# Performance work log

Measured on AMD Instinct MI355X. Metric: run time of the kernel, lower is better.

The kernel has to match this reference:

```python
import jax, jax.numpy as jnp
import numpy as np

D, H, F, N, V, B, S, T = 512, 8, 2048, 2, 32000, 2, 1024, 1024


def _pe(seq_len, d):
    pos = np.arange(seq_len)[:, None].astype(np.float32)
    div = np.exp(np.arange(0, d, 2).astype(np.float32) * (-np.log(10000.0) / d))
    pe = np.zeros((seq_len, d), np.float32)
    pe[:, 0::2] = np.sin(pos * div)
    pe[:, 1::2] = np.cos(pos * div)
    return jnp.asarray(pe)


def _ln(x, g, b, eps=1e-6):
    # torch .var() default is unbiased (ddof=1)
    m = x.mean(-1, keepdims=True)
    v = jnp.sum((x - m) ** 2, -1, keepdims=True) / (x.shape[-1] - 1)
    return g * (x - m) / jnp.sqrt(v + eps) + b


def _mha(q, k, v, mask, w, b):
    # w: [4, D, D] (q,k,v,o); b: [4, D]
    Bq, Sq, Dm = q.shape
    Sk = k.shape[1]
    dk = Dm // H
    Q = (q @ w[0] + b[0]).reshape(Bq, Sq, H, dk).transpose(0, 2, 1, 3)
    K = (k @ w[1] + b[1]).reshape(Bq, Sk, H, dk).transpose(0, 2, 1, 3)
    Vv = (v @ w[2] + b[2]).reshape(Bq, Sk, H, dk).transpose(0, 2, 1, 3)
    s = jnp.einsum('bhqd,bhkd->bhqk', Q, K) / jnp.sqrt(jnp.float32(dk))
    s = jnp.where(mask == 0, jnp.float32(-1e9), s)
    a = jax.nn.softmax(s, axis=-1)
    o = jnp.einsum('bhqk,bhkd->bhqd', a, Vv).transpose(0, 2, 1, 3).reshape(Bq, Sq, Dm)
    return o @ w[3] + b[3]


def _ffn(x, w1, b1, w2, b2):
    return jax.nn.relu(x @ w1 + b1) @ w2 + b2


def _forward(src, tgt, src_mask, tgt_mask, p):
    (src_emb, tgt_emb, ea_w, ea_b, ef_w1, ef_b1, ef_w2, ef_b2, eln_g, eln_b, en_g, en_b,
     ds_w, ds_b, dc_w, dc_b, df_w1, df_b1, df_w2, df_b2, dln_g, dln_b, dn_g, dn_b, pw, pb) = p
    scale = jnp.sqrt(jnp.float32(D))
    # encoder
    x = src_emb[src] * scale + _pe(src.shape[1], D)
    for i in range(N):
        h = _ln(x, eln_g[i, 0], eln_b[i, 0])
        x = x + _mha(h, h, h, src_mask, ea_w[i], ea_b[i])
        h = _ln(x, eln_g[i, 1], eln_b[i, 1])
        x = x + _ffn(h, ef_w1[i], ef_b1[i], ef_w2[i], ef_b2[i])
    enc = _ln(x, en_g, en_b)
    # decoder
    y = tgt_emb[tgt] * scale + _pe(tgt.shape[1], D)
    for i in range(N):
        h = _ln(y, dln_g[i, 0], dln_b[i, 0])
        y = y + _mha(h, h, h, tgt_mask, ds_w[i], ds_b[i])
        h = _ln(y, dln_g[i, 1], dln_b[i, 1])
        y = y + _mha(h, enc, enc, src_mask, dc_w[i], dc_b[i])
        h = _ln(y, dln_g[i, 2], dln_b[i, 2])
        y = y + _ffn(h, df_w1[i], df_b1[i], df_w2[i], df_b2[i])
    y = _ln(y, dn_g, dn_b)
    return jax.nn.log_softmax(y @ pw + pb, axis=-1)


def setup_inputs() -> dict:
    key = jax.random.key(0)
    c = [0]
    def nk():
        c[0] += 1
        return jax.random.fold_in(key, c[0])
    def w(*s):
        return jax.random.normal(nk(), s, jnp.float32) * 0.02
    inp = {
        'src': jax.random.randint(nk(), (B, S), 0, V, jnp.int32),
        'tgt': jax.random.randint(nk(), (B, T), 0, V, jnp.int32),
        'src_mask': jnp.ones((B, 1, 1, S), jnp.int32),
        'tgt_mask': jnp.tril(jnp.ones((T, T), jnp.int32))[None, None],
        'src_emb': w(V, D), 'tgt_emb': w(V, D),
        'enc_attn_w': w(N, 4, D, D), 'enc_attn_b': jnp.zeros((N, 4, D), jnp.float32),
        'enc_ffn_w1': w(N, D, F), 'enc_ffn_b1': jnp.zeros((N, F), jnp.float32),
        'enc_ffn_w2': w(N, F, D), 'enc_ffn_b2': jnp.zeros((N, D), jnp.float32),
        'enc_ln_g': jnp.ones((N, 2, D), jnp.float32), 'enc_ln_b': jnp.zeros((N, 2, D), jnp.float32),
        'enc_norm_g': jnp.ones((D,), jnp.float32), 'enc_norm_b': jnp.zeros((D,), jnp.float32),
        'dec_self_w': w(N, 4, D, D), 'dec_self_b': jnp.zeros((N, 4, D), jnp.float32),
        'dec_cross_w': w(N, 4, D, D), 'dec_cross_b': jnp.zeros((N, 4, D), jnp.float32),
        'dec_ffn_w1': w(N, D, F), 'dec_ffn_b1': jnp.zeros((N, F), jnp.float32),
        'dec_ffn_w2': w(N, F, D), 'dec_ffn_b2': jnp.zeros((N, D), jnp.float32),
        'dec_ln_g': jnp.ones((N, 3, D), jnp.float32), 'dec_ln_b': jnp.zeros((N, 3, D), jnp.float32),
        'dec_norm_g': jnp.ones((D,), jnp.float32), 'dec_norm_b': jnp.zeros((D,), jnp.float32),
        'proj_w': w(D, V), 'proj_b': jnp.zeros((V,), jnp.float32),
    }
    return inp


def reference(src, tgt, src_mask, tgt_mask, src_emb, tgt_emb, enc_attn_w, enc_attn_b,
              enc_ffn_w1, enc_ffn_b1, enc_ffn_w2, enc_ffn_b2, enc_ln_g, enc_ln_b,
              enc_norm_g, enc_norm_b, dec_self_w, dec_self_b, dec_cross_w, dec_cross_b,
              dec_ffn_w1, dec_ffn_b1, dec_ffn_w2, dec_ffn_b2, dec_ln_g, dec_ln_b,
              dec_norm_g, dec_norm_b, proj_w, proj_b):
    p = (src_emb, tgt_emb, enc_attn_w, enc_attn_b, enc_ffn_w1, enc_ffn_b1, enc_ffn_w2,
         enc_ffn_b2, enc_ln_g, enc_ln_b, enc_norm_g, enc_norm_b, dec_self_w, dec_self_b,
         dec_cross_w, dec_cross_b, dec_ffn_w1, dec_ffn_b1, dec_ffn_w2, dec_ffn_b2,
         dec_ln_g, dec_ln_b, dec_norm_g, dec_norm_b, proj_w, proj_b)
    return _forward(src, tgt, src_mask, tgt_mask, p)
```

## Files before the change

### kernel.cpp

```cpp
#include <hip/hip_runtime.h>
#include <hip/hip_bf16.h>
#include <math.h>

using bf16 = __hip_bfloat16;
typedef float f32x4 __attribute__((ext_vector_type(4)));
typedef short short8 __attribute__((ext_vector_type(8)));

constexpr int kD = 512, kH = 8, kDk = 64, kF = 2048, kV = 32000;
constexpr int kB = 2, kS = 1024, kM = 2048, kBH = 16;

enum { ST_F32 = 0, ST_BF16, ST_QHEAD, ST_QKV, ST_KV };

__device__ __forceinline__ void gload_lds16(const void* g, void* l) {
  __builtin_amdgcn_global_load_lds(
      (const __attribute__((address_space(1))) void*)g,
      (__attribute__((address_space(3))) void*)l, 16, 0, 0);
}

template <int BM, int BN, int STM, bool BIAS, bool RELU, bool RES, bool DBUF, bool XSWZ>
__launch_bounds__(256)
__global__ void k_gemm(const bf16* __restrict__ A, int lda, long long Az,
                       const bf16* __restrict__ Bt, int ldb, long long Bz,
                       void* __restrict__ Cv, int ldc, long long Cz,
                       int K, float alpha,
                       const float* __restrict__ bias,
                       const float* __restrict__ res) {
  static_assert(!DBUF || (BM == 64 && BN == 64), "DBUF path sized for 64x64 (vmcnt(4))");
  constexpr int FM = BM / 32, FN = BN / 32;
  constexpr int NB = DBUF ? 2 : 1;
  __shared__ __attribute__((aligned(16))) bf16 As[NB][BM * 64];
  __shared__ __attribute__((aligned(16))) bf16 Bs[NB][BN * 64];
  const int tid = threadIdx.x;
  const int w = tid >> 6, lane = tid & 63;
  int bx = blockIdx.x, by = blockIdx.y;
  if constexpr (XSWZ) {
    const int nx = gridDim.x;
    const int lin = by * nx + bx;
    const int cpx = (nx * gridDim.y) >> 3;
    const int s = (lin & 7) * cpx + (lin >> 3);
    bx = s % nx;
    by = s / nx;
  }
  const int bm = by * BM, bn = bx * BN;
  const int z = blockIdx.z;
  A += (long long)z * Az;
  Bt += (long long)z * Bz;
  const int l15 = lane & 15, lhi = lane >> 4;
  const int wr = (w >> 1) * (BM / 2), wc = (w & 1) * (BN / 2);
  f32x4 acc[FM][FN] = {};
  const int nkt = K >> 6;

  auto stage = [&](int kt, int nb) {
#pragma unroll
    for (int it = 0; it < BM / 32; ++it) {
      int chunk = (it * 4 + w) * 64 + lane;
      int row = chunk >> 3, col = (chunk & 7) << 3;
      gload_lds16(A + (size_t)(bm + row) * lda + kt * 64 + col, As[nb] + (it * 4 + w) * 512);
    }
#pragma unroll
    for (int it = 0; it < BN / 32; ++it) {
      int chunk = (it * 4 + w) * 64 + lane;
      int row = chunk >> 3, col = (chunk & 7) << 3;
      gload_lds16(Bt + (size_t)(bn + row) * ldb + kt * 64 + col, Bs[nb] + (it * 4 + w) * 512);
    }
  };
  auto compute = [&](int cb) {
#pragma unroll
    for (int kk = 0; kk < 2; ++kk) {
      short8 af[FM], bf[FN];
#pragma unroll
      for (int i = 0; i < FM; ++i)
        af[i] = *(const short8*)(As[cb] + (wr + i * 16 + l15) * 64 + kk * 32 + lhi * 8);
#pragma unroll
      for (int j = 0; j < FN; ++j)
        bf[j] = *(const short8*)(Bs[cb] + (wc + j * 16 + l15) * 64 + kk * 32 + lhi * 8);
#pragma unroll
      for (int i = 0; i < FM; ++i)
#pragma unroll
        for (int j = 0; j < FN; ++j)
          acc[i][j] = __builtin_amdgcn_mfma_f32_16x16x32_bf16(af[i], bf[j], acc[i][j], 0, 0, 0);
    }
  };

  if constexpr (DBUF) {
    stage(0, 0);
    stage(1, 1);
    asm volatile("s_waitcnt vmcnt(4)" ::: "memory");
    __builtin_amdgcn_s_barrier();
    __builtin_amdgcn_sched_barrier(0);
    int cur = 0;
    for (int kt = 0; kt < nkt; ++kt) {
      compute(cur);
      asm volatile("s_waitcnt lgkmcnt(0)" ::: "memory");
      __builtin_amdgcn_sched_barrier(0);
      if (kt + 1 < nkt) {
        __builtin_amdgcn_s_barrier();
        if (kt + 2 < nkt) {
          stage(kt + 2, cur);
          asm volatile("s_waitcnt vmcnt(4)" ::: "memory");
        } else {
          asm volatile("s_waitcnt vmcnt(0)" ::: "memory");
        }
        __builtin_amdgcn_s_barrier();
        __builtin_amdgcn_sched_barrier(0);
      }
      cur ^= 1;
    }
  } else {
    for (int kt = 0; kt < nkt; ++kt) {
      stage(kt, 0);
      __syncthreads();
      compute(0);
      __syncthreads();
    }
  }

#pragma unroll
  for (int i = 0; i < FM; ++i) {
#pragma unroll
    for (int j = 0; j < FN; ++j) {
#pragma unroll
      for (int r = 0; r < 4; ++r) {
        int m = bm + wr + i * 16 + lhi * 4 + r;
        int n = bn + wc + j * 16 + l15;
        float val = acc[i][j][r] * alpha;
        if constexpr (BIAS) val += bias[n];
        if constexpr (RELU) val = fmaxf(val, 0.f);
        if constexpr (RES) val += res[(size_t)m * ldc + n];
        if constexpr (STM == ST_F32) {
          ((float*)Cv)[(size_t)z * Cz + (size_t)m * ldc + n] = val;
        } else if constexpr (STM == ST_BF16) {
          ((bf16*)Cv)[(size_t)z * Cz + (size_t)m * ldc + n] = __float2bfloat16(val);
        } else if constexpr (STM == ST_QHEAD) {
          int b_ = m >> 10, s_ = m & 1023, h_ = n >> 6, d_ = n & 63;
          ((bf16*)Cv)[(((size_t)(b_ * kH + h_) << 10) + s_) * kDk + d_] = __float2bfloat16(val);
        } else if constexpr (STM == ST_QKV) {
          int seg = n >> 9, nn = n & 511;
          int b_ = m >> 10, s_ = m & 1023, h_ = nn >> 6, d_ = nn & 63;
          size_t idx = (seg < 2)
              ? (((size_t)(b_ * kH + h_) << 10) + s_) * kDk + d_
              : ((size_t)(b_ * kH + h_) * kDk + d_) * kS + s_;
          ((bf16*)Cv)[(size_t)seg * 1048576 + idx] = __float2bfloat16(val);
        } else if constexpr (STM == ST_KV) {
          int seg = n >> 9, nn = n & 511;
          int b_ = m >> 10, s_ = m & 1023, h_ = nn >> 6, d_ = nn & 63;
          size_t idx = (seg == 0)
              ? (((size_t)(b_ * kH + h_) << 10) + s_) * kDk + d_
              : ((size_t)(b_ * kH + h_) * kDk + d_) * kS + s_;
          ((bf16*)Cv)[(size_t)(seg + 1) * 1048576 + idx] = __float2bfloat16(val);
        }
      }
    }
  }
}

template <bool CAUSAL>
__launch_bounds__(256)
__global__ void k_fattn(const bf16* __restrict__ Q, const bf16* __restrict__ K,
                        const bf16* __restrict__ Vt, bf16* __restrict__ O) {
  __shared__ __attribute__((aligned(16))) bf16 Ks[2][4096];
  __shared__ __attribute__((aligned(16))) bf16 Vs[2][4096];
  __shared__ __attribute__((aligned(16))) bf16 Ps[4][1024];
  const int tid = threadIdx.x, w = tid >> 6, lane = tid & 63;
  const int l15 = lane & 15, lhi = lane >> 4;
  const int q0 = blockIdx.x * 64, bh = blockIdx.y;
  const int qw = q0 + w * 16;
  const bf16* Qp = Q + (((size_t)(bh << 10)) + qw + l15) * kDk;
  short8 aq[2];
  aq[0] = *(const short8*)(Qp + lhi * 8);
  aq[1] = *(const short8*)(Qp + 32 + lhi * 8);
  const int srow = w * 8 + (lane >> 3);
  const int sc = (lane & 7) ^ (srow & 7);
  const bf16* Ksrc = K + (((size_t)(bh << 10)) + srow) * kDk + sc * 8;
  const bf16* Vsrc = Vt + ((size_t)bh * kDk + srow) * kS + sc * 8;
  const int nt = CAUSAL ? (q0 >> 6) + 1 : (kS >> 6);

  auto stage = [&](int t, int nb) {
    int kv0 = t << 6;
    gload_lds16(Ksrc + (size_t)kv0 * kDk, Ks[nb] + w * 512);
    gload_lds16(Ksrc + (size_t)(kv0 + 32) * kDk, Ks[nb] + 2048 + w * 512);
    gload_lds16(Vsrc + kv0, Vs[nb] + w * 512);
    gload_lds16(Vsrc + kv0 + 32 * kS, Vs[nb] + 2048 + w * 512);
  };

  float m_[4], l_[4];
#pragma unroll
  for (int r = 0; r < 4; ++r) { m_[r] = -1e30f; l_[r] = 0.f; }
  f32x4 ao[4] = {};

  stage(0, 0);
  if (nt > 1) {
    stage(1, 1);
    asm volatile("s_waitcnt vmcnt(4)" ::: "memory");
  } else {
    asm volatile("s_waitcnt vmcnt(0)" ::: "memory");
  }
  __builtin_amdgcn_s_barrier();
  __builtin_amdgcn_sched_barrier(0);

  for (int t = 0; t < nt; ++t) {
    const int cur = t & 1;
    f32x4 as[4] = {};
#pragma unroll
    for (int kk = 0; kk < 2; ++kk) {
      short8 bk[4];
#pragma unroll
      for (int nf = 0; nf < 4; ++nf) {
        int row = nf * 16 + l15;
        int c = (4 * kk + lhi) ^ (row & 7);
        bk[nf] = *(const short8*)(Ks[cur] + row * 64 + c * 8);
      }
#pragma unroll
      for (int nf = 0; nf < 4; ++nf)
        as[nf] = __builtin_amdgcn_mfma_f32_16x16x32_bf16(aq[kk], bk[nf], as[nf], 0, 0, 0);
    }
    float s[4][4];
#pragma unroll
    for (int nf = 0; nf < 4; ++nf)
#pragma unroll
      for (int r = 0; r < 4; ++r) {
        float v = as[nf][r] * 0.125f;
        if (CAUSAL && t == nt - 1) {
          int col = (t << 6) + nf * 16 + l15;
          int row = qw + lhi * 4 + r;
          if (col > row) v = -1e30f;
        }
        s[nf][r] = v;
      }
    float mn[4], scl[4], rsum[4];
#pragma unroll
    for (int r = 0; r < 4; ++r) {
      float mx = fmaxf(fmaxf(s[0][r], s[1][r]), fmaxf(s[2][r], s[3][r]));
      mx = fmaxf(mx, __shfl_xor(mx, 1));
      mx = fmaxf(mx, __shfl_xor(mx, 2));
      mx = fmaxf(mx, __shfl_xor(mx, 4));
      mx = fmaxf(mx, __shfl_xor(mx, 8));
      mn[r] = fmaxf(m_[r], mx);
      scl[r] = __expf(m_[r] - mn[r]);
      rsum[r] = 0.f;
    }
#pragma unroll
    for (int nf = 0; nf < 4; ++nf)
#pragma unroll
      for (int r = 0; r < 4; ++r) {
        float p = __expf(s[nf][r] - mn[r]);
        rsum[r] += p;
        int pr = lhi * 4 + r;
        int c = (2 * nf + (l15 >> 3)) ^ (pr & 7);
        Ps[w][pr * 64 + c * 8 + (l15 & 7)] = __float2bfloat16(p);
      }
#pragma unroll
    for (int r = 0; r < 4; ++r) {
      float su = rsum[r];
      su += __shfl_xor(su, 1);
      su += __shfl_xor(su, 2);
      su += __shfl_xor(su, 4);
      su += __shfl_xor(su, 8);
      l_[r] = l_[r] * scl[r] + su;
      m_[r] = mn[r];
    }
#pragma unroll
    for (int nf = 0; nf < 4; ++nf)
#pragma unroll
      for (int r = 0; r < 4; ++r) ao[nf][r] *= scl[r];
    asm volatile("s_waitcnt lgkmcnt(0)" ::: "memory");
    __builtin_amdgcn_sched_barrier(0);
#pragma unroll
    for (int kk = 0; kk < 2; ++kk) {
      short8 pa = *(const short8*)(Ps[w] + l15 * 64 + (((4 * kk + lhi) ^ (l15 & 7)) * 8));
      short8 bv[4];
#pragma unroll
      for (int nf = 0; nf < 4; ++nf) {
        int row = nf * 16 + l15;
        int c = (4 * kk + lhi) ^ (row & 7);
        bv[nf] = *(const short8*)(Vs[cur] + row * 64 + c * 8);
      }
#pragma unroll
      for (int nf = 0; nf < 4; ++nf)
        ao[nf] = __builtin_amdgcn_mfma_f32_16x16x32_bf16(pa, bv[nf], ao[nf], 0, 0, 0);
    }
    asm volatile("s_waitcnt lgkmcnt(0)" ::: "memory");
    __builtin_amdgcn_sched_barrier(0);
    if (t + 1 < nt) {
      __builtin_amdgcn_s_barrier();
      if (t + 2 < nt) {
        stage(t + 2, cur);
        asm volatile("s_waitcnt vmcnt(4)" ::: "memory");
      } else {
        asm volatile("s_waitcnt vmcnt(0)" ::: "memory");
      }
      __builtin_amdgcn_s_barrier();
      __builtin_amdgcn_sched_barrier(0);
    }
  }
  const int b_ = bh >> 3, h_ = bh & 7;
  float inv[4];
#pragma unroll
  for (int r = 0; r < 4; ++r) inv[r] = 1.f / l_[r];
#pragma unroll
  for (int nf = 0; nf < 4; ++nf)
#pragma unroll
    for (int r = 0; r < 4; ++r) {
      int q = qw + lhi * 4 + r;
      O[((size_t)(b_ * kS + q)) * kD + h_ * kDk + nf * 16 + l15] =
          __float2bfloat16(ao[nf][r] * inv[r]);
    }
}

struct TJobs {
  const float* src[8];
  bf16* dst[8];
  int K[8], N[8];
  int ofs[9];
};

__global__ void k_transpose_all(TJobs J) {
  __shared__ float t[32][33];
  const int tb = blockIdx.x;
  int j = 0;
#pragma unroll
  for (int i = 1; i < 8; ++i) j += (tb >= J.ofs[i]) ? 1 : 0;
  const int K = J.K[j], N = J.N[j];
  const int tn = N >> 5, tk = K >> 5;
  int r = tb - J.ofs[j];
  const int z = r / (tn * tk);
  r -= z * tn * tk;
  const int k0 = (r / tn) << 5, n0 = (r % tn) << 5;
  const float* Wp = J.src[j] + (size_t)z * K * N;
  bf16* WTp = J.dst[j] + (size_t)z * K * N;
  const int tx = threadIdx.x, ty = threadIdx.y;
#pragma unroll
  for (int rr = 0; rr < 32; rr += 8) t[ty + rr][tx] = Wp[(size_t)(k0 + ty + rr) * N + n0 + tx];
  __syncthreads();
#pragma unroll
  for (int rr = 0; rr < 32; rr += 8)
    WTp[(size_t)(n0 + ty + rr) * K + k0 + tx] = __float2bfloat16(t[tx][ty + rr]);
}

__global__ void k_embed(const int* __restrict__ tok, const float* __restrict__ emb,
                        float* __restrict__ x) {
  int m = blockIdx.x;
  int s = m & (kS - 1);
  const float* e = emb + (size_t)tok[m] * kD;
  float* xp = x + (size_t)m * kD;
  for (int d = threadIdx.x; d < kD; d += 256) {
    int i = d >> 1;
    float freq = __expf(-(float)(2 * i) * (9.210340371976184f / 512.0f));
    float ang = (float)s * freq;
    float pe = (d & 1) ? cosf(ang) : sinf(ang);
    xp[d] = e[d] * 22.62741699796952f + pe;
  }
}

__global__ void k_ln(const float* __restrict__ x, const float* __restrict__ g,
                     const float* __restrict__ b, bf16* __restrict__ out) {
  int w = threadIdx.x >> 6, lane = threadIdx.x & 63;
  int row = blockIdx.x * 4 + w;
  const float* xp = x + (size_t)row * kD;
  float v[8];
  float sum = 0.f;
#pragma unroll
  for (int i = 0; i < 8; ++i) { v[i] = xp[lane + i * 64]; sum += v[i]; }
#pragma unroll
  for (int o = 32; o; o >>= 1) sum += __shfl_xor(sum, o);
  float mean = sum * (1.f / 512.f);
  float sq = 0.f;
#pragma unroll
  for (int i = 0; i < 8; ++i) { float d = v[i] - mean; sq += d * d; }
#pragma unroll
  for (int o = 32; o; o >>= 1) sq += __shfl_xor(sq, o);
  float inv = rsqrtf(sq * (1.f / 511.f) + 1e-6f);
  bf16* op = out + (size_t)row * kD;
#pragma unroll
  for (int i = 0; i < 8; ++i) {
    int d = lane + i * 64;
    op[d] = __float2bfloat16(g[d] * (v[i] - mean) * inv + b[d]);
  }
}

__global__ __launch_bounds__(640, 2) void k_logsoftmax(float* __restrict__ y) {
  float* row = y + (size_t)blockIdx.x * kV;
  const int t = threadIdx.x;
  float v[50];
  float mx = -1e30f;
#pragma unroll
  for (int i = 0; i < 50; ++i) { v[i] = row[t + i * 640]; mx = fmaxf(mx, v[i]); }
#pragma unroll
  for (int o = 32; o; o >>= 1) mx = fmaxf(mx, __shfl_xor(mx, o));
  __shared__ float red[10], red2[10];
  const int w = t >> 6, lane = t & 63;
  if (lane == 0) red[w] = mx;
  __syncthreads();
#pragma unroll
  for (int i = 0; i < 10; ++i) mx = fmaxf(mx, red[i]);
  float sum = 0.f;
#pragma unroll
  for (int i = 0; i < 50; ++i) { v[i] -= mx; sum += __expf(v[i]); }
#pragma unroll
  for (int o = 32; o; o >>= 1) sum += __shfl_xor(sum, o);
  if (lane == 0) red2[w] = sum;
  __syncthreads();
  sum = 0.f;
#pragma unroll
  for (int i = 0; i < 10; ++i) sum += red2[i];
  const float ls = logf(sum);
#pragma unroll
  for (int i = 0; i < 50; ++i) row[t + i * 640] = v[i] - ls;
}

extern "C" void kernel_launch(void* const* d_in, const int* in_sizes, int n_in,
                              void* d_out, int out_size, void* d_ws, size_t ws_size,
                              hipStream_t stream) {
  (void)in_sizes; (void)n_in; (void)out_size;
  if (ws_size < (size_t)80 * 1024 * 1024) return;

  const int* src = (const int*)d_in[0];
  const int* tgt = (const int*)d_in[1];
  const float* src_emb   = (const float*)d_in[4];
  const float* tgt_emb   = (const float*)d_in[5];
  const float* enc_attn_w = (const float*)d_in[6];
  const float* enc_attn_b = (const float*)d_in[7];
  const float* enc_ffn_w1 = (const float*)d_in[8];
  const float* enc_ffn_b1 = (const float*)d_in[9];
  const float* enc_ffn_w2 = (const float*)d_in[10];
  const float* enc_ffn_b2 = (const float*)d_in[11];
  const float* enc_ln_g  = (const float*)d_in[12];
  const float* enc_ln_b  = (const float*)d_in[13];
  const float* enc_norm_g = (const float*)d_in[14];
  const float* enc_norm_b = (const float*)d_in[15];
  const float* dec_self_w = (const float*)d_in[16];
  const float* dec_self_b = (const float*)d_in[17];
  const float* dec_cross_w = (const float*)d_in[18];
  const float* dec_cross_b = (const float*)d_in[19];
  const float* dec_ffn_w1 = (const float*)d_in[20];
  const float* dec_ffn_b1 = (const float*)d_in[21];
  const float* dec_ffn_w2 = (const float*)d_in[22];
  const float* dec_ffn_b2 = (const float*)d_in[23];
  const float* dec_ln_g  = (const float*)d_in[24];
  const float* dec_ln_b  = (const float*)d_in[25];
  const float* dec_norm_g = (const float*)d_in[26];
  const float* dec_norm_b = (const float*)d_in[27];
  const float* proj_w    = (const float*)d_in[28];
  const float* proj_b    = (const float*)d_in[29];

  char* ws = (char*)d_ws;
  auto MB = [](size_t x) { return x << 20; };
  bf16* enc_attn_wt  = (bf16*)(ws + MB(0));
  bf16* dec_self_wt  = (bf16*)(ws + MB(4));
  bf16* dec_cross_wt = (bf16*)(ws + MB(8));
  bf16* enc_f1t = (bf16*)(ws + MB(12));
  bf16* enc_f2t = (bf16*)(ws + MB(16));
  bf16* dec_f1t = (bf16*)(ws + MB(20));
  bf16* dec_f2t = (bf16*)(ws + MB(24));
  bf16* proj_wt = (bf16*)(ws + MB(28));
  float* x_enc  = (float*)(ws + MB(60));
  float* x_dec  = (float*)(ws + MB(64));
  bf16* hbuf    = (bf16*)(ws + MB(68));
  bf16* enc_bf  = (bf16*)(ws + MB(70));
  bf16* Qb      = (bf16*)(ws + MB(72));
  bf16* Kb      = (bf16*)(ws + MB(74));
  bf16* VtB     = (bf16*)(ws + MB(76));
  bf16* attn_o  = (bf16*)(ws + MB(78));
  bf16* ffn_mid = (bf16*)d_out;

  TJobs tj;
  int acc = 0;
  auto setj = [&](int j, const float* s, bf16* d, int K, int N, int z) {
    tj.src[j] = s; tj.dst[j] = d; tj.K[j] = K; tj.N[j] = N; tj.ofs[j] = acc;
    acc += (K >> 5) * (N >> 5) * z;
  };
  setj(0, enc_attn_w, enc_attn_wt, 512, 512, 8);
  setj(1, dec_self_w, dec_self_wt, 512, 512, 8);
  setj(2, dec_cross_w, dec_cross_wt, 512, 512, 8);
  setj(3, enc_ffn_w1, enc_f1t, 512, 2048, 2);
  setj(4, enc_ffn_w2, enc_f2t, 2048, 512, 2);
  setj(5, dec_ffn_w1, dec_f1t, 512, 2048, 2);
  setj(6, dec_ffn_w2, dec_f2t, 2048, 512, 2);
  setj(7, proj_w, proj_wt, 512, 32000, 1);
  tj.ofs[8] = acc;
  k_transpose_all<<<acc, dim3(32, 8), 0, stream>>>(tj);

  k_embed<<<kM, 256, 0, stream>>>(src, src_emb, x_enc);
  k_embed<<<kM, 256, 0, stream>>>(tgt, tgt_emb, x_dec);

  auto LN = [&](const float* x, const float* g, const float* b, bf16* out) {
    k_ln<<<kM / 4, 256, 0, stream>>>(x, g, b, out);
  };
  auto out_proj = [&](const bf16* wt, const float* bias, float* xio) {
    k_gemm<64, 64, ST_F32, true, false, true, true, false><<<dim3(8, 32, 1), 256, 0, stream>>>(
        attn_o, 512, 0, wt + 3 * 262144, 512, 0, xio, 512, 0, 512, 1.f, bias + 3 * 512, xio);
  };
  auto self_attn = [&](const bf16* wt, const float* bias, bool causal, float* xio) {
    k_gemm<64, 64, ST_QKV, true, false, false, true, false><<<dim3(24, 32, 1), 256, 0, stream>>>(
        hbuf, 512, 0, wt, 512, 0, Qb, 0, 0, 512, 1.f, bias, nullptr);
    if (causal) k_fattn<true><<<dim3(16, kBH), 256, 0, stream>>>(Qb, Kb, VtB, attn_o);
    else        k_fattn<false><<<dim3(16, kBH), 256, 0, stream>>>(Qb, Kb, VtB, attn_o);
    out_proj(wt, bias, xio);
  };
  auto cross_attn = [&](const bf16* wt, const float* bias, float* xio) {
    k_gemm<64, 64, ST_QHEAD, true, false, false, true, false><<<dim3(8, 32, 1), 256, 0, stream>>>(
        hbuf, 512, 0, wt, 512, 0, Qb, 0, 0, 512, 1.f, bias, nullptr);
    k_gemm<64, 64, ST_KV, true, false, false, true, false><<<dim3(16, 32, 1), 256, 0, stream>>>(
        enc_bf, 512, 0, wt + 1 * 262144, 512, 0, Qb, 0, 0, 512, 1.f, bias + 512, nullptr);
    k_fattn<false><<<dim3(16, kBH), 256, 0, stream>>>(Qb, Kb, VtB, attn_o);
    out_proj(wt, bias, xio);
  };
  auto ffn_block = [&](float* xio, const bf16* w1t, const float* b1, const bf16* w2t,
                       const float* b2, const float* g, const float* bl) {
    LN(xio, g, bl, hbuf);
    k_gemm<128, 128, ST_BF16, true, true, false, false, false><<<dim3(16, 16, 1), 256, 0, stream>>>(
        hbuf, 512, 0, w1t, 512, 0, ffn_mid, 2048, 0, 512, 1.f, b1, nullptr);
    k_gemm<64, 64, ST_F32, true, false, true, true, false><<<dim3(8, 32, 1), 256, 0, stream>>>(
        ffn_mid, 2048, 0, w2t, 2048, 0, xio, 512, 0, 2048, 1.f, b2, xio);
  };

  for (int i = 0; i < 2; ++i) {
    LN(x_enc, enc_ln_g + i * 1024, enc_ln_b + i * 1024, hbuf);
    self_attn(enc_attn_wt + (size_t)i * 1048576, enc_attn_b + i * 2048, false, x_enc);
    ffn_block(x_enc, enc_f1t + (size_t)i * 1048576, enc_ffn_b1 + i * 2048,
              enc_f2t + (size_t)i * 1048576, enc_ffn_b2 + i * 512,
              enc_ln_g + i * 1024 + 512, enc_ln_b + i * 1024 + 512);
  }
  LN(x_enc, enc_norm_g, enc_norm_b, enc_bf);

  for (int i = 0; i < 2; ++i) {
    LN(x_dec, dec_ln_g + i * 1536, dec_ln_b + i * 1536, hbuf);
    self_attn(dec_self_wt + (size_t)i * 1048576, dec_self_b + i * 2048, true, x_dec);
    LN(x_dec, dec_ln_g + i * 1536 + 512, dec_ln_b + i * 1536 + 512, hbuf);
    cross_attn(dec_cross_wt + (size_t)i * 1048576, dec_cross_b + i * 2048, x_dec);
    ffn_block(x_dec, dec_f1t + (size_t)i * 1048576, dec_ffn_b1 + i * 2048,
              dec_f2t + (size_t)i * 1048576, dec_ffn_b2 + i * 512,
              dec_ln_g + i * 1536 + 1024, dec_ln_b + i * 1536 + 1024);
  }
  LN(x_dec, dec_norm_g, dec_norm_b, hbuf);

  k_gemm<128, 128, ST_F32, true, false, false, false, true><<<dim3(250, 16, 1), 256, 0, stream>>>(
      hbuf, 512, 0, proj_wt, 512, 0, (float*)d_out, kV, 0, 512, 1.f, proj_b, nullptr);
  k_logsoftmax<<<kM, 640, 0, stream>>>((float*)d_out);
}
```

Baseline: 797.0 us.

## Fuse LayerNorm into projection GEMMs and store logits as bf16

Adds a GEMM kernel that computes LayerNorm on the fp32 residual rows inside the block and keeps the full 64x512 normalized A tile in LDS. This removes the separate LN launches and the hbuf round trip. Cross-attention Q and K/V projections become one launch, where the K/V column blocks copy the precomputed encoder bf16 rows. The vocab projection now writes bf16 logits to workspace and log-softmax reads them back vectorized, halving the intermediate traffic at the cost of bf16 rounding of logits and a larger workspace requirement.

```diff
diff --git a/kernel.cpp b/kernel.cpp
--- a/kernel.cpp
+++ b/kernel.cpp
@@ -9,12 +9,18 @@
 constexpr int kD = 512, kH = 8, kDk = 64, kF = 2048, kV = 32000;
 constexpr int kB = 2, kS = 1024, kM = 2048, kBH = 16;
 
-enum { ST_F32 = 0, ST_BF16, ST_QHEAD, ST_QKV, ST_KV };
+enum { ST_F32 = 0, ST_BF16, ST_QKV };
 
 __device__ __forceinline__ void gload_lds16(const void* g, void* l) {
   __builtin_amdgcn_global_load_lds(
       (const __attribute__((address_space(1))) void*)g,
       (__attribute__((address_space(3))) void*)l, 16, 0, 0);
+}
+
+__device__ __forceinline__ float bfu2f(short u) {
+  union { unsigned int i; float f; } c;
+  c.i = ((unsigned int)(unsigned short)u) << 16;
+  return c.f;
 }
 
 template <int BM, int BN, int STM, bool BIAS, bool RELU, bool RES, bool DBUF, bool XSWZ>
@@ -131,23 +137,142 @@
           ((float*)Cv)[(size_t)z * Cz + (size_t)m * ldc + n] = val;
         } else if constexpr (STM == ST_BF16) {
           ((bf16*)Cv)[(size_t)z * Cz + (size_t)m * ldc + n] = __float2bfloat16(val);
-        } else if constexpr (STM == ST_QHEAD) {
-          int b_ = m >> 10, s_ = m & 1023, h_ = n >> 6, d_ = n & 63;
-          ((bf16*)Cv)[(((size_t)(b_ * kH + h_) << 10) + s_) * kDk + d_] = __float2bfloat16(val);
-        } else if constexpr (STM == ST_QKV) {
+        }
+      }
+    }
+  }
+}
+
+template <int BN, int STM, bool RELU, bool CROSS>
+__launch_bounds__(256)
+__global__ void k_gemm_lnf(const float* __restrict__ Af, const float* __restrict__ g,
+                           const float* __restrict__ bv, const bf16* __restrict__ Ab,
+                           const bf16* __restrict__ Bt,
+                           void* __restrict__ Cv, int ldc,
+                           const float* __restrict__ bias) {
+  constexpr int FM = 2, FN = BN / 32, SB = BN / 32;
+  __shared__ __attribute__((aligned(16))) bf16 As2[64 * 512];
+  __shared__ __attribute__((aligned(16))) bf16 Bs[2][BN * 64];
+  const int tid = threadIdx.x;
+  const int w = tid >> 6, lane = tid & 63;
+  const int l15 = lane & 15, lhi = lane >> 4;
+  const int bm = blockIdx.y * 64, bn = blockIdx.x * BN;
+  const int wr = (w >> 1) * 32, wc = (w & 1) * (BN / 2);
+
+  {
+    const int r = tid >> 2, q = tid & 3;
+    const bool docopy = CROSS && (bn >= 512);
+    if (!docopy) {
+      const float* xr = Af + (size_t)(bm + r) * kD + q * 128;
+      float sum = 0.f, ss = 0.f;
+#pragma unroll
+      for (int i = 0; i < 32; ++i) {
+        f32x4 v = *(const f32x4*)(xr + i * 4);
+        sum += v[0] + v[1] + v[2] + v[3];
+        ss += v[0] * v[0] + v[1] * v[1] + v[2] * v[2] + v[3] * v[3];
+      }
+      sum += __shfl_xor(sum, 1); sum += __shfl_xor(sum, 2);
+      ss  += __shfl_xor(ss, 1);  ss  += __shfl_xor(ss, 2);
+      const float mean = sum * (1.f / 512.f);
+      const float rstd = rsqrtf((ss - sum * mean) * (1.f / 511.f) + 1e-6f);
+#pragma unroll
+      for (int j = 0; j < 16; ++j) {
+        short8 o;
+#pragma unroll
+        for (int h = 0; h < 2; ++h) {
+          f32x4 xv = *(const f32x4*)(xr + j * 8 + h * 4);
+          f32x4 gv = *(const f32x4*)(g + q * 128 + j * 8 + h * 4);
+          f32x4 bvv = *(const f32x4*)(bv + q * 128 + j * 8 + h * 4);
+#pragma unroll
+          for (int e = 0; e < 4; ++e) {
+            bf16 t = __float2bfloat16(gv[e] * (xv[e] - mean) * rstd + bvv[e]);
+            o[h * 4 + e] = *(short*)&t;
+          }
+        }
+        *(short8*)(As2 + r * 512 + (((q * 16 + j) ^ (r & 7)) * 8)) = o;
+      }
+    } else {
+      const bf16* ar = Ab + (size_t)(bm + r) * kD + q * 128;
+#pragma unroll
+      for (int j = 0; j < 16; ++j)
+        *(short8*)(As2 + r * 512 + (((q * 16 + j) ^ (r & 7)) * 8)) =
+            *(const short8*)(ar + j * 8);
+    }
+  }
+
+  auto stageB = [&](int kt, int nb) {
+#pragma unroll
+    for (int it = 0; it < SB; ++it) {
+      int chunk = (it * 4 + w) * 64 + lane;
+      int row = chunk >> 3, col = (chunk & 7) << 3;
+      gload_lds16(Bt + (size_t)(bn + row) * kD + kt * 64 + col, Bs[nb] + (it * 4 + w) * 512);
+    }
+  };
+
+  f32x4 acc[FM][FN] = {};
+  stageB(0, 0);
+  stageB(1, 1);
+  asm volatile("s_waitcnt lgkmcnt(0)" ::: "memory");
+  __builtin_amdgcn_s_barrier();
+  if constexpr (SB == 2) asm volatile("s_waitcnt vmcnt(2)" ::: "memory");
+  else                   asm volatile("s_waitcnt vmcnt(4)" ::: "memory");
+  __builtin_amdgcn_sched_barrier(0);
+
+  for (int kt = 0; kt < 8; ++kt) {
+    const int cur = kt & 1;
+#pragma unroll
+    for (int kk = 0; kk < 2; ++kk) {
+      short8 af[FM], bf[FN];
+#pragma unroll
+      for (int i = 0; i < FM; ++i) {
+        int row = wr + i * 16 + l15;
+        int c = kt * 8 + kk * 4 + lhi;
+        af[i] = *(const short8*)(As2 + row * 512 + ((c ^ (row & 7)) * 8));
+      }
+#pragma unroll
+      for (int j = 0; j < FN; ++j)
+        bf[j] = *(const short8*)(Bs[cur] + (wc + j * 16 + l15) * 64 + kk * 32 + lhi * 8);
+#pragma unroll
+      for (int i = 0; i < FM; ++i)
+#pragma unroll
+        for (int j = 0; j < FN; ++j)
+          acc[i][j] = __builtin_amdgcn_mfma_f32_16x16x32_bf16(af[i], bf[j], acc[i][j], 0, 0, 0);
+    }
+    asm volatile("s_waitcnt lgkmcnt(0)" ::: "memory");
+    __builtin_amdgcn_sched_barrier(0);
+    if (kt < 7) {
+      __builtin_amdgcn_s_barrier();
+      if (kt < 6) {
+        stageB(kt + 2, cur);
+        if constexpr (SB == 2) asm volatile("s_waitcnt vmcnt(2)" ::: "memory");
+        else                   asm volatile("s_waitcnt vmcnt(4)" ::: "memory");
+      } else {
+        asm volatile("s_waitcnt vmcnt(0)" ::: "memory");
+      }
+      __builtin_amdgcn_s_barrier();
+      __builtin_amdgcn_sched_barrier(0);
+    }
+  }
+
+#pragma unroll
+  for (int i = 0; i < FM; ++i) {
+#pragma unroll
+    for (int j = 0; j < FN; ++j) {
+#pragma unroll
+      for (int r = 0; r < 4; ++r) {
+        int m = bm + wr + i * 16 + lhi * 4 + r;
+        int n = bn + wc + j * 16 + l15;
+        float val = acc[i][j][r] + bias[n];
+        if constexpr (RELU) val = fmaxf(val, 0.f);
+        if constexpr (STM == ST_BF16) {
+          ((bf16*)Cv)[(size_t)m * ldc + n] = __float2bfloat16(val);
+        } else {
           int seg = n >> 9, nn = n & 511;
           int b_ = m >> 10, s_ = m & 1023, h_ = nn >> 6, d_ = nn & 63;
           size_t idx = (seg < 2)
               ? (((size_t)(b_ * kH + h_) << 10) + s_) * kDk + d_
               : ((size_t)(b_ * kH + h_) * kDk + d_) * kS + s_;
           ((bf16*)Cv)[(size_t)seg * 1048576 + idx] = __float2bfloat16(val);
-        } else if constexpr (STM == ST_KV) {
-          int seg = n >> 9, nn = n & 511;
-          int b_ = m >> 10, s_ = m & 1023, h_ = nn >> 6, d_ = nn & 63;
-          size_t idx = (seg == 0)
-              ? (((size_t)(b_ * kH + h_) << 10) + s_) * kDk + d_
-              : ((size_t)(b_ * kH + h_) * kDk + d_) * kS + s_;
-          ((bf16*)Cv)[(size_t)(seg + 1) * 1048576 + idx] = __float2bfloat16(val);
         }
       }
     }
@@ -378,13 +503,36 @@
   }
 }
 
-__global__ __launch_bounds__(640, 2) void k_logsoftmax(float* __restrict__ y) {
-  float* row = y + (size_t)blockIdx.x * kV;
+__global__ __launch_bounds__(640, 2) void k_lsm_bf(const bf16* __restrict__ L,
+                                                   float* __restrict__ y) {
+  const bf16* row = L + (size_t)blockIdx.x * kV;
+  float* orow = y + (size_t)blockIdx.x * kV;
   const int t = threadIdx.x;
-  float v[50];
+  const bool extra = t < 160;
+  float v[56];
   float mx = -1e30f;
 #pragma unroll
-  for (int i = 0; i < 50; ++i) { v[i] = row[t + i * 640]; mx = fmaxf(mx, v[i]); }
+  for (int i = 0; i < 6; ++i) {
+    short8 s = *(const short8*)(row + (t + i * 640) * 8);
+#pragma unroll
+    for (int e = 0; e < 8; ++e) {
+      float f = bfu2f(s[e]);
+      v[i * 8 + e] = f;
+      mx = fmaxf(mx, f);
+    }
+  }
+  if (extra) {
+    short8 s = *(const short8*)(row + (3840 + t) * 8);
+#pragma unroll
+    for (int e = 0; e < 8; ++e) {
+      float f = bfu2f(s[e]);
+      v[48 + e] = f;
+      mx = fmaxf(mx, f);
+    }
+  } else {
+#pragma unroll
+    for (int e = 0; e < 8; ++e) v[48 + e] = -1e30f;
+  }
 #pragma unroll
   for (int o = 32; o; o >>= 1) mx = fmaxf(mx, __shfl_xor(mx, o));
   __shared__ float red[10], red2[10];
@@ -395,7 +543,7 @@
   for (int i = 0; i < 10; ++i) mx = fmaxf(mx, red[i]);
   float sum = 0.f;
 #pragma unroll
-  for (int i = 0; i < 50; ++i) { v[i] -= mx; sum += __expf(v[i]); }
+  for (int i = 0; i < 56; ++i) sum += __expf(v[i] - mx);
 #pragma unroll
   for (int o = 32; o; o >>= 1) sum += __shfl_xor(sum, o);
   if (lane == 0) red2[w] = sum;
@@ -403,16 +551,21 @@
   sum = 0.f;
 #pragma unroll
   for (int i = 0; i < 10; ++i) sum += red2[i];
-  const float ls = logf(sum);
-#pragma unroll
-  for (int i = 0; i < 50; ++i) row[t + i * 640] = v[i] - ls;
+  const float sh = mx + logf(sum);
+#pragma unroll
+  for (int i = 0; i < 6; ++i)
+#pragma unroll
+    for (int e = 0; e < 8; ++e) orow[(t + i * 640) * 8 + e] = v[i * 8 + e] - sh;
+  if (extra)
+#pragma unroll
+    for (int e = 0; e < 8; ++e) orow[(3840 + t) * 8 + e] = v[48 + e] - sh;
 }
 
 extern "C" void kernel_launch(void* const* d_in, const int* in_sizes, int n_in,
                               void* d_out, int out_size, void* d_ws, size_t ws_size,
                               hipStream_t stream) {
   (void)in_sizes; (void)n_in; (void)out_size;
-  if (ws_size < (size_t)80 * 1024 * 1024) return;
+  if (ws_size < (size_t)212 * 1024 * 1024) return;
 
   const int* src = (const int*)d_in[0];
   const int* tgt = (const int*)d_in[1];
@@ -461,6 +614,7 @@
   bf16* Kb      = (bf16*)(ws + MB(74));
   bf16* VtB     = (bf16*)(ws + MB(76));
   bf16* attn_o  = (bf16*)(ws + MB(78));
+  bf16* logits  = (bf16*)(ws + MB(80));
   bf16* ffn_mid = (bf16*)d_out;
 
   TJobs tj;
@@ -483,58 +637,54 @@
   k_embed<<<kM, 256, 0, stream>>>(src, src_emb, x_enc);
   k_embed<<<kM, 256, 0, stream>>>(tgt, tgt_emb, x_dec);
 
-  auto LN = [&](const float* x, const float* g, const float* b, bf16* out) {
-    k_ln<<<kM / 4, 256, 0, stream>>>(x, g, b, out);
-  };
   auto out_proj = [&](const bf16* wt, const float* bias, float* xio) {
     k_gemm<64, 64, ST_F32, true, false, true, true, false><<<dim3(8, 32, 1), 256, 0, stream>>>(
         attn_o, 512, 0, wt + 3 * 262144, 512, 0, xio, 512, 0, 512, 1.f, bias + 3 * 512, xio);
   };
-  auto self_attn = [&](const bf16* wt, const float* bias, bool causal, float* xio) {
-    k_gemm<64, 64, ST_QKV, true, false, false, true, false><<<dim3(24, 32, 1), 256, 0, stream>>>(
-        hbuf, 512, 0, wt, 512, 0, Qb, 0, 0, 512, 1.f, bias, nullptr);
+  auto self_attn = [&](const bf16* wt, const float* bias, const float* lg, const float* lb,
+                       bool causal, float* xio) {
+    k_gemm_lnf<64, ST_QKV, false, false><<<dim3(24, 32), 256, 0, stream>>>(
+        xio, lg, lb, nullptr, wt, Qb, 0, bias);
     if (causal) k_fattn<true><<<dim3(16, kBH), 256, 0, stream>>>(Qb, Kb, VtB, attn_o);
     else        k_fattn<false><<<dim3(16, kBH), 256, 0, stream>>>(Qb, Kb, VtB, attn_o);
     out_proj(wt, bias, xio);
   };
-  auto cross_attn = [&](const bf16* wt, const float* bias, float* xio) {
-    k_gemm<64, 64, ST_QHEAD, true, false, false, true, false><<<dim3(8, 32, 1), 256, 0, stream>>>(
-        hbuf, 512, 0, wt, 512, 0, Qb, 0, 0, 512, 1.f, bias, nullptr);
-    k_gemm<64, 64, ST_KV, true, false, false, true, false><<<dim3(16, 32, 1), 256, 0, stream>>>(
-        enc_bf, 512, 0, wt + 1 * 262144, 512, 0, Qb, 0, 0, 512, 1.f, bias + 512, nullptr);
+  auto cross_attn = [&](const bf16* wt, const float* bias, const float* lg, const float* lb,
+                        float* xio) {
+    k_gemm_lnf<64, ST_QKV, false, true><<<dim3(24, 32), 256, 0, stream>>>(
+        xio, lg, lb, enc_bf, wt, Qb, 0, bias);
     k_fattn<false><<<dim3(16, kBH), 256, 0, stream>>>(Qb, Kb, VtB, attn_o);
     out_proj(wt, bias, xio);
   };
   auto ffn_block = [&](float* xio, const bf16* w1t, const float* b1, const bf16* w2t,
-                       const float* b2, const float* g, const float* bl) {
-    LN(xio, g, bl, hbuf);
-    k_gemm<128, 128, ST_BF16, true, true, false, false, false><<<dim3(16, 16, 1), 256, 0, stream>>>(
-        hbuf, 512, 0, w1t, 512, 0, ffn_mid, 2048, 0, 512, 1.f, b1, nullptr);
+                       const float* b2, const float* lg, const float* lb) {
+    k_gemm_lnf<128, ST_BF16, true, false><<<dim3(16, 32), 256, 0, stream>>>(
+        xio, lg, lb, nullptr, w1t, ffn_mid, kF, b1);
     k_gemm<64, 64, ST_F32, true, false, true, true, false><<<dim3(8, 32, 1), 256, 0, stream>>>(
         ffn_mid, 2048, 0, w2t, 2048, 0, xio, 512, 0, 2048, 1.f, b2, xio);
   };
 
   for (int i = 0; i < 2; ++i) {
-    LN(x_enc, enc_ln_g + i * 1024, enc_ln_b + i * 1024, hbuf);
-    self_attn(enc_attn_wt + (size_t)i * 1048576, enc_attn_b + i * 2048, false, x_enc);
+    self_attn(enc_attn_wt + (size_t)i * 1048576, enc_attn_b + i * 2048,
+              enc_ln_g + i * 1024, enc_ln_b + i * 1024, false, x_enc);
     ffn_block(x_enc, enc_f1t + (size_t)i * 1048576, enc_ffn_b1 + i * 2048,
               enc_f2t + (size_t)i * 1048576, enc_ffn_b2 + i * 512,
               enc_ln_g + i * 1024 + 512, enc_ln_b + i * 1024 + 512);
   }
-  LN(x_enc, enc_norm_g, enc_norm_b, enc_bf);
+  k_ln<<<kM / 4, 256, 0, stream>>>(x_enc, enc_norm_g, enc_norm_b, enc_bf);
 
   for (int i = 0; i < 2; ++i) {
-    LN(x_dec, dec_ln_g + i * 1536, dec_ln_b + i * 1536, hbuf);
-    self_attn(dec_self_wt + (size_t)i * 1048576, dec_self_b + i * 2048, true, x_dec);
-    LN(x_dec, dec_ln_g + i * 1536 + 512, dec_ln_b + i * 1536 + 512, hbuf);
-    cross_attn(dec_cross_wt + (size_t)i * 1048576, dec_cross_b + i * 2048, x_dec);
+    self_attn(dec_self_wt + (size_t)i * 1048576, dec_self_b + i * 2048,
+              dec_ln_g + i * 1536, dec_ln_b + i * 1536, true, x_dec);
+    cross_attn(dec_cross_wt + (size_t)i * 1048576, dec_cross_b + i * 2048,
+               dec_ln_g + i * 1536 + 512, dec_ln_b + i * 1536 + 512, x_dec);
     ffn_block(x_dec, dec_f1t + (size_t)i * 1048576, dec_ffn_b1 + i * 2048,
               dec_f2t + (size_t)i * 1048576, dec_ffn_b2 + i * 512,
               dec_ln_g + i * 1536 + 1024, dec_ln_b + i * 1536 + 1024);
   }
-  LN(x_dec, dec_norm_g, dec_norm_b, hbuf);
-
-  k_gemm<128, 128, ST_F32, true, false, false, false, true><<<dim3(250, 16, 1), 256, 0, stream>>>(
-      hbuf, 512, 0, proj_wt, 512, 0, (float*)d_out, kV, 0, 512, 1.f, proj_b, nullptr);
-  k_logsoftmax<<<kM, 640, 0, stream>>>((float*)d_out);
-}
+  k_ln<<<kM / 4, 256, 0, stream>>>(x_dec, dec_norm_g, dec_norm_b, hbuf);
+
+  k_gemm<128, 128, ST_BF16, true, false, false, false, true><<<dim3(250, 16, 1), 256, 0, stream>>>(
+      hbuf, 512, 0, proj_wt, 512, 0, logits, kV, 0, 512, 1.f, proj_b, nullptr);
+  k_lsm_bf<<<kM, 640, 0, stream>>>(logits, (float*)d_out);
+}
```

New measurement: 976.1 us. +22.5%, slower.

## Store projection logits in bf16 and vectorize log-softmax reads

Applied to the files above, without the earlier changes.

The vocab projection GEMM now writes bf16 logits to a workspace buffer instead of fp32 logits into the output. A new log-softmax kernel reads those logits with 16-byte vector loads and writes the fp32 result, which roughly halves the intermediate write and read traffic. The XSWZ block swizzle is also changed to walk column-major over tiles, which alters L2 reuse in the projection GEMM. In exchange, the logits are rounded to bf16 before softmax, which costs some precision, and the workspace requirement grows considerably.

```diff
diff --git a/kernel.cpp b/kernel.cpp
--- a/kernel.cpp
+++ b/kernel.cpp
@@ -15,6 +15,12 @@
   __builtin_amdgcn_global_load_lds(
       (const __attribute__((address_space(1))) void*)g,
       (__attribute__((address_space(3))) void*)l, 16, 0, 0);
+}
+
+__device__ __forceinline__ float bfu2f(short u) {
+  union { unsigned int i; float f; } c;
+  c.i = ((unsigned int)(unsigned short)u) << 16;
+  return c.f;
 }
 
 template <int BM, int BN, int STM, bool BIAS, bool RELU, bool RES, bool DBUF, bool XSWZ>
@@ -34,12 +40,12 @@
   const int w = tid >> 6, lane = tid & 63;
   int bx = blockIdx.x, by = blockIdx.y;
   if constexpr (XSWZ) {
-    const int nx = gridDim.x;
+    const int nx = gridDim.x, ny = gridDim.y;
     const int lin = by * nx + bx;
-    const int cpx = (nx * gridDim.y) >> 3;
+    const int cpx = (nx * ny) >> 3;
     const int s = (lin & 7) * cpx + (lin >> 3);
-    bx = s % nx;
-    by = s / nx;
+    bx = s / ny;
+    by = s - bx * ny;
   }
   const int bm = by * BM, bn = bx * BN;
   const int z = blockIdx.z;
@@ -378,13 +384,36 @@
   }
 }
 
-__global__ __launch_bounds__(640, 2) void k_logsoftmax(float* __restrict__ y) {
-  float* row = y + (size_t)blockIdx.x * kV;
+__global__ __launch_bounds__(640, 2) void k_lsm_bf(const bf16* __restrict__ L,
+                                                   float* __restrict__ y) {
+  const bf16* row = L + (size_t)blockIdx.x * kV;
+  float* orow = y + (size_t)blockIdx.x * kV;
   const int t = threadIdx.x;
-  float v[50];
+  const bool extra = t < 160;
+  float v[56];
   float mx = -1e30f;
 #pragma unroll
-  for (int i = 0; i < 50; ++i) { v[i] = row[t + i * 640]; mx = fmaxf(mx, v[i]); }
+  for (int i = 0; i < 6; ++i) {
+    short8 s = *(const short8*)(row + (t + i * 640) * 8);
+#pragma unroll
+    for (int e = 0; e < 8; ++e) {
+      float f = bfu2f(s[e]);
+      v[i * 8 + e] = f;
+      mx = fmaxf(mx, f);
+    }
+  }
+  if (extra) {
+    short8 s = *(const short8*)(row + (3840 + t) * 8);
+#pragma unroll
+    for (int e = 0; e < 8; ++e) {
+      float f = bfu2f(s[e]);
+      v[48 + e] = f;
+      mx = fmaxf(mx, f);
+    }
+  } else {
+#pragma unroll
+    for (int e = 0; e < 8; ++e) v[48 + e] = -1e30f;
+  }
 #pragma unroll
   for (int o = 32; o; o >>= 1) mx = fmaxf(mx, __shfl_xor(mx, o));
   __shared__ float red[10], red2[10];
@@ -395,7 +424,7 @@
   for (int i = 0; i < 10; ++i) mx = fmaxf(mx, red[i]);
   float sum = 0.f;
 #pragma unroll
-  for (int i = 0; i < 50; ++i) { v[i] -= mx; sum += __expf(v[i]); }
+  for (int i = 0; i < 56; ++i) sum += __expf(v[i] - mx);
 #pragma unroll
   for (int o = 32; o; o >>= 1) sum += __shfl_xor(sum, o);
   if (lane == 0) red2[w] = sum;
@@ -403,16 +432,21 @@
   sum = 0.f;
 #pragma unroll
   for (int i = 0; i < 10; ++i) sum += red2[i];
-  const float ls = logf(sum);
-#pragma unroll
-  for (int i = 0; i < 50; ++i) row[t + i * 640] = v[i] - ls;
+  const float sh = mx + logf(sum);
+#pragma unroll
+  for (int i = 0; i < 6; ++i)
+#pragma unroll
+    for (int e = 0; e < 8; ++e) orow[(t + i * 640) * 8 + e] = v[i * 8 + e] - sh;
+  if (extra)
+#pragma unroll
+    for (int e = 0; e < 8; ++e) orow[(3840 + t) * 8 + e] = v[48 + e] - sh;
 }
 
 extern "C" void kernel_launch(void* const* d_in, const int* in_sizes, int n_in,
                               void* d_out, int out_size, void* d_ws, size_t ws_size,
                               hipStream_t stream) {
   (void)in_sizes; (void)n_in; (void)out_size;
-  if (ws_size < (size_t)80 * 1024 * 1024) return;
+  if (ws_size < (size_t)212 * 1024 * 1024) return;
 
   const int* src = (const int*)d_in[0];
   const int* tgt = (const int*)d_in[1];
@@ -461,6 +495,7 @@
   bf16* Kb      = (bf16*)(ws + MB(74));
   bf16* VtB     = (bf16*)(ws + MB(76));
   bf16* attn_o  = (bf16*)(ws + MB(78));
+  bf16* logits  = (bf16*)(ws + MB(80));
   bf16* ffn_mid = (bf16*)d_out;
 
   TJobs tj;
@@ -534,7 +569,7 @@
   }
   LN(x_dec, dec_norm_g, dec_norm_b, hbuf);
 
-  k_gemm<128, 128, ST_F32, true, false, false, false, true><<<dim3(250, 16, 1), 256, 0, stream>>>(
-      hbuf, 512, 0, proj_wt, 512, 0, (float*)d_out, kV, 0, 512, 1.f, proj_b, nullptr);
-  k_logsoftmax<<<kM, 640, 0, stream>>>((float*)d_out);
-}
+  k_gemm<128, 128, ST_BF16, true, false, false, false, true><<<dim3(250, 16, 1), 256, 0, stream>>>(
+      hbuf, 512, 0, proj_wt, 512, 0, logits, kV, 0, 512, 1.f, proj_b, nullptr);
+  k_lsm_bf<<<kM, 640, 0, stream>>>(logits, (float*)d_out);
+}
```

After: 759.0 us. 1.05x faster.
